# Kernel optimization log

Measured on AMD Instinct MI355X. Metric: run time of the kernel, lower is better.

The kernel has to match this reference:

```python
import jax, jax.numpy as jnp
import numpy as np

N, E = 20000, 200000
DIM, EDGE_DIM, HID = 128, 64, 256


def _linear_init(key, fan_in, fan_out):
    # torch nn.Linear default: U(-1/sqrt(fan_in), 1/sqrt(fan_in)) for W and b
    kw, kb = jax.random.split(key)
    bound = 1.0 / np.sqrt(fan_in)
    W = jax.random.uniform(kw, (fan_in, fan_out), minval=-bound, maxval=bound, dtype=jnp.float32)
    b = jax.random.uniform(kb, (fan_out,), minval=-bound, maxval=bound, dtype=jnp.float32)
    return W, b


def setup_inputs() -> dict:
    key = jax.random.key(0)
    ks = jax.random.split(key, 8)
    H = jax.random.normal(ks[0], (N, DIM), dtype=jnp.float32)
    src = jax.random.randint(ks[1], (E,), 0, N, dtype=jnp.int32)
    dst = jax.random.randint(ks[2], (E,), 0, N, dtype=jnp.int32)
    edge_index = jnp.stack([src, dst], axis=0)
    edge_attr = jax.random.normal(ks[3], (E, EDGE_DIM), dtype=jnp.float32)
    msg_W1, msg_b1 = _linear_init(ks[4], DIM + EDGE_DIM, HID)
    msg_W2, msg_b2 = _linear_init(ks[5], HID, DIM)
    self_W1, self_b1 = _linear_init(ks[6], DIM, HID)
    self_W2, self_b2 = _linear_init(ks[7], HID, DIM)
    eps = jnp.zeros((1,), dtype=jnp.float32)
    return dict(H=H, edge_index=edge_index, edge_attr=edge_attr, eps=eps,
                msg_W1=msg_W1, msg_b1=msg_b1, msg_W2=msg_W2, msg_b2=msg_b2,
                self_W1=self_W1, self_b1=self_b1, self_W2=self_W2, self_b2=self_b2)


def _mlp(x, W1, b1, W2, b2):
    h = jax.nn.relu(x @ W1 + b1)
    return h @ W2 + b2


def reference(H, edge_index, edge_attr, eps,
              msg_W1, msg_b1, msg_W2, msg_b2,
              self_W1, self_b1, self_W2, self_b2):
    src, dst = edge_index[0], edge_index[1]
    # gather source node features, concat edge features -> per-edge message MLP
    msg_in = jnp.concatenate([H[src], edge_attr], axis=-1)  # [E, dim+edge_dim]
    msg = _mlp(msg_in, msg_W1, msg_b1, msg_W2, msg_b2)       # [E, dim]
    # scatter-add messages to destination nodes
    agg = jax.ops.segment_sum(msg, dst, num_segments=H.shape[0])  # [N, dim]
    return _mlp((1.0 + eps) * H + agg, self_W1, self_b1, self_W2, self_b2)
```

## Files before the change

kernel.cpp:

```cpp
#include <hip/hip_runtime.h>

typedef float  f32x4  __attribute__((ext_vector_type(4)));
typedef short  bf16x8 __attribute__((ext_vector_type(8)));
typedef unsigned short u16;

#define NN   20000
#define NE   200000
#define DIM  128
#define EDIM 64
#define HID  256
#define KIN  192

__device__ __forceinline__ u16 f2b(float f) {
  unsigned u = __float_as_uint(f);
  u += 0x7FFFu + ((u >> 16) & 1u);
  return (u16)(u >> 16);
}

__global__ void prep_kernel(const float* __restrict__ mW1, const float* __restrict__ mW2,
                            const float* __restrict__ sW1, const float* __restrict__ sW2,
                            u16* __restrict__ W1T, u16* __restrict__ W2T,
                            u16* __restrict__ S1T, u16* __restrict__ S2T) {
  int t  = blockIdx.x * blockDim.x + threadIdx.x;
  int nt = gridDim.x * blockDim.x;
  for (int i = t; i < KIN * HID; i += nt) { int k = i / HID, n = i % HID; W1T[n * KIN + k] = f2b(mW1[i]); }
  for (int i = t; i < HID * DIM; i += nt) { int k = i / DIM, n = i % DIM; W2T[n * HID + k] = f2b(mW2[i]); }
  for (int i = t; i < DIM * HID; i += nt) { int k = i / HID, n = i % HID; S1T[n * DIM + k] = f2b(sW1[i]); }
  for (int i = t; i < HID * DIM; i += nt) { int k = i / DIM, n = i % DIM; S2T[n * HID + k] = f2b(sW2[i]); }
}

__global__ void hist_kernel(const int* __restrict__ EI, int* __restrict__ cnt) {
  int i = blockIdx.x * 256 + threadIdx.x;
  if (i < NE) atomicAdd(&cnt[EI[NE + i]], 1);
}

__global__ __launch_bounds__(1024) void scan_kernel(const int* __restrict__ cnt,
                                                    int* __restrict__ cursor) {
  __shared__ int ls[1024];
  const int t = threadIdx.x;
  const int base = t * 20;
  int v[20]; int s = 0;
  #pragma unroll
  for (int j = 0; j < 20; ++j) {
    int idx = base + j;
    int c = (idx < NN) ? cnt[idx] : 0;
    v[j] = s; s += c;
  }
  ls[t] = s;
  __syncthreads();
  for (int off = 1; off < 1024; off <<= 1) {
    int x = (t >= off) ? ls[t - off] : 0;
    __syncthreads();
    ls[t] += x;
    __syncthreads();
  }
  int boff = (t > 0) ? ls[t - 1] : 0;
  #pragma unroll
  for (int j = 0; j < 20; ++j) {
    int idx = base + j;
    if (idx < NN) cursor[idx] = boff + v[j];
  }
}

__global__ void scatter_kernel(const int* __restrict__ EI, int* __restrict__ cursor,
                               int* __restrict__ perm, int* __restrict__ srcs,
                               int* __restrict__ dsts) {
  int i = blockIdx.x * 256 + threadIdx.x;
  if (i < NE) {
    int d = EI[NE + i];
    int pos = atomicAdd(&cursor[d], 1);
    perm[pos] = i;
    srcs[pos] = EI[i];
    dsts[pos] = d;
  }
}

__global__ __launch_bounds__(256, 4) void edge_kernel(
    const float* __restrict__ H, const float* __restrict__ EA,
    const int* __restrict__ perm, const int* __restrict__ srcs,
    const int* __restrict__ dsts,
    const u16* __restrict__ W1T, const float* __restrict__ b1p,
    const u16* __restrict__ W2T, const float* __restrict__ b2p,
    float* __restrict__ agg) {
  __shared__ int src_s[64];
  __shared__ int eid_s[64];
  __shared__ int dst_s[64];
  __shared__ u16 smem[64 * HID];

  const int tid = threadIdx.x;
  const int e0  = blockIdx.x * 64;
  if (tid < 64) {
    src_s[tid] = srcs[e0 + tid];
    eid_s[tid] = perm[e0 + tid];
    dst_s[tid] = dsts[e0 + tid];
  }
  __syncthreads();

  #pragma unroll
  for (int i = 0; i < 8; ++i) {
    int idx = tid + i * 256;
    int row = idx >> 5, c4 = idx & 31;
    const float4 v = reinterpret_cast<const float4*>(H + (size_t)src_s[row] * DIM)[c4];
    int by = (c4 * 8) ^ ((row & 7) << 4);
    ushort4 o; o.x = f2b(v.x); o.y = f2b(v.y); o.z = f2b(v.z); o.w = f2b(v.w);
    *reinterpret_cast<ushort4*>(&smem[row * KIN + (by >> 1)]) = o;
  }
  #pragma unroll
  for (int i = 0; i < 4; ++i) {
    int idx = tid + i * 256;
    int row = idx >> 4, c4 = idx & 15;
    const float4 v = reinterpret_cast<const float4*>(EA + (size_t)eid_s[row] * EDIM)[c4];
    int by = (256 + c4 * 8) ^ ((row & 7) << 4);
    ushort4 o; o.x = f2b(v.x); o.y = f2b(v.y); o.z = f2b(v.z); o.w = f2b(v.w);
    *reinterpret_cast<ushort4*>(&smem[row * KIN + (by >> 1)]) = o;
  }
  __syncthreads();

  const int wv = tid >> 6, lane = tid & 63;
  const int lr = lane & 15, lg = lane >> 4;
  const f32x4 zero = {0.f, 0.f, 0.f, 0.f};

  const int n0 = wv * 64;
  f32x4 acc[4][4];
  #pragma unroll
  for (int m = 0; m < 4; ++m)
    #pragma unroll
    for (int n = 0; n < 4; ++n) acc[m][n] = zero;
  float bias1[4];
  #pragma unroll
  for (int n = 0; n < 4; ++n) bias1[n] = b1p[n0 + n * 16 + lr];

  #pragma unroll
  for (int kt = 0; kt < 6; ++kt) {
    bf16x8 af[4], bf[4];
    #pragma unroll
    for (int m = 0; m < 4; ++m) {
      int row = m * 16 + lr;
      int by  = (kt * 64 + lg * 16) ^ ((row & 7) << 4);
      af[m] = *reinterpret_cast<const bf16x8*>(&smem[row * KIN + (by >> 1)]);
    }
    #pragma unroll
    for (int n = 0; n < 4; ++n) {
      int nabs = n0 + n * 16 + lr;
      bf[n] = *reinterpret_cast<const bf16x8*>(&W1T[nabs * KIN + kt * 32 + lg * 8]);
    }
    #pragma unroll
    for (int m = 0; m < 4; ++m)
      #pragma unroll
      for (int n = 0; n < 4; ++n)
        acc[m][n] = __builtin_amdgcn_mfma_f32_16x16x32_bf16(af[m], bf[n], acc[m][n], 0, 0, 0);
  }
  __syncthreads();

  #pragma unroll
  for (int m = 0; m < 4; ++m)
    #pragma unroll
    for (int n = 0; n < 4; ++n)
      #pragma unroll
      for (int r = 0; r < 4; ++r) {
        int row = m * 16 + lg * 4 + r;
        int col = n0 + n * 16 + lr;
        float v = acc[m][n][r] + bias1[n];
        v = fmaxf(v, 0.0f);
        int by = (col * 2) ^ ((row & 7) << 4);
        smem[row * HID + (by >> 1)] = f2b(v);
      }
  __syncthreads();

  const int n0b = wv * 32;
  f32x4 acc2[4][2];
  #pragma unroll
  for (int m = 0; m < 4; ++m) { acc2[m][0] = zero; acc2[m][1] = zero; }
  float bias2[2];
  #pragma unroll
  for (int n = 0; n < 2; ++n) bias2[n] = b2p[n0b + n * 16 + lr];

  #pragma unroll
  for (int kt = 0; kt < 8; ++kt) {
    bf16x8 af[4], bf[2];
    #pragma unroll
    for (int m = 0; m < 4; ++m) {
      int row = m * 16 + lr;
      int by  = (kt * 64 + lg * 16) ^ ((row & 7) << 4);
      af[m] = *reinterpret_cast<const bf16x8*>(&smem[row * HID + (by >> 1)]);
    }
    #pragma unroll
    for (int n = 0; n < 2; ++n) {
      int nabs = n0b + n * 16 + lr;
      bf[n] = *reinterpret_cast<const bf16x8*>(&W2T[nabs * HID + kt * 32 + lg * 8]);
    }
    #pragma unroll
    for (int m = 0; m < 4; ++m)
      #pragma unroll
      for (int n = 0; n < 2; ++n)
        acc2[m][n] = __builtin_amdgcn_mfma_f32_16x16x32_bf16(af[m], bf[n], acc2[m][n], 0, 0, 0);
  }
  __syncthreads();

  float* msgf = reinterpret_cast<float*>(smem);
  #pragma unroll
  for (int m = 0; m < 4; ++m)
    #pragma unroll
    for (int n = 0; n < 2; ++n) {
      float bb = bias2[n];
      int col = n0b + n * 16 + lr;
      #pragma unroll
      for (int r = 0; r < 4; ++r) {
        int row = m * 16 + lg * 4 + r;
        msgf[row * DIM + (col ^ ((row & 7) << 2))] = acc2[m][n][r] + bb;
      }
    }
  __syncthreads();

  if (tid < DIM) {
    const int c = tid;
    float s = 0.f;
    int cur = dst_s[0];
    int seg0 = 0;
    for (int r = 0; r < 64; ++r) {
      int d = dst_s[r];
      if (d != cur) {
        if (seg0 == 0) atomicAdd(&agg[(size_t)cur * DIM + c], s);
        else           agg[(size_t)cur * DIM + c] = s;
        s = 0.f; cur = d; seg0 = r;
      }
      s += msgf[r * DIM + (c ^ ((r & 7) << 2))];
    }
    atomicAdd(&agg[(size_t)cur * DIM + c], s);
  }
}

__global__ __launch_bounds__(256, 6) void self_kernel(
    const float* __restrict__ H, const float* __restrict__ agg,
    const float* __restrict__ epsp,
    const u16* __restrict__ S1T, const float* __restrict__ b1p,
    const u16* __restrict__ S2T, const float* __restrict__ b2p,
    float* __restrict__ out) {
  __shared__ u16 smem[32 * HID];
  const int tid = threadIdx.x;
  const int r0  = blockIdx.x * 32;
  const float sc = 1.0f + epsp[0];

  #pragma unroll
  for (int i = 0; i < 4; ++i) {
    int idx = tid + i * 256;
    int row = idx >> 5, c4 = idx & 31;
    int gr = r0 + row;
    const float4 h = reinterpret_cast<const float4*>(H   + (size_t)gr * DIM)[c4];
    const float4 a = reinterpret_cast<const float4*>(agg + (size_t)gr * DIM)[c4];
    ushort4 o;
    o.x = f2b(sc * h.x + a.x); o.y = f2b(sc * h.y + a.y);
    o.z = f2b(sc * h.z + a.z); o.w = f2b(sc * h.w + a.w);
    int by = (c4 * 8) ^ ((row & 7) << 4);
    *reinterpret_cast<ushort4*>(&smem[row * DIM + (by >> 1)]) = o;
  }
  __syncthreads();

  const int wv = tid >> 6, lane = tid & 63;
  const int lr = lane & 15, lg = lane >> 4;
  const f32x4 zero = {0.f, 0.f, 0.f, 0.f};

  const int n0 = wv * 64;
  f32x4 acc[2][4];
  #pragma unroll
  for (int m = 0; m < 2; ++m)
    #pragma unroll
    for (int n = 0; n < 4; ++n) acc[m][n] = zero;
  float bias1[4];
  #pragma unroll
  for (int n = 0; n < 4; ++n) bias1[n] = b1p[n0 + n * 16 + lr];

  #pragma unroll
  for (int kt = 0; kt < 4; ++kt) {
    bf16x8 af[2], bf[4];
    #pragma unroll
    for (int m = 0; m < 2; ++m) {
      int row = m * 16 + lr;
      int by  = (kt * 64 + lg * 16) ^ ((row & 7) << 4);
      af[m] = *reinterpret_cast<const bf16x8*>(&smem[row * DIM + (by >> 1)]);
    }
    #pragma unroll
    for (int n = 0; n < 4; ++n) {
      int nabs = n0 + n * 16 + lr;
      bf[n] = *reinterpret_cast<const bf16x8*>(&S1T[nabs * DIM + kt * 32 + lg * 8]);
    }
    #pragma unroll
    for (int m = 0; m < 2; ++m)
      #pragma unroll
      for (int n = 0; n < 4; ++n)
        acc[m][n] = __builtin_amdgcn_mfma_f32_16x16x32_bf16(af[m], bf[n], acc[m][n], 0, 0, 0);
  }
  __syncthreads();

  #pragma unroll
  for (int m = 0; m < 2; ++m)
    #pragma unroll
    for (int n = 0; n < 4; ++n)
      #pragma unroll
      for (int r = 0; r < 4; ++r) {
        int row = m * 16 + lg * 4 + r;
        int col = n0 + n * 16 + lr;
        float v = acc[m][n][r] + bias1[n];
        v = fmaxf(v, 0.0f);
        int by = (col * 2) ^ ((row & 7) << 4);
        smem[row * HID + (by >> 1)] = f2b(v);
      }
  __syncthreads();

  const int n0b = wv * 32;
  f32x4 acc2[2][2];
  #pragma unroll
  for (int m = 0; m < 2; ++m) { acc2[m][0] = zero; acc2[m][1] = zero; }
  float bias2[2];
  #pragma unroll
  for (int n = 0; n < 2; ++n) bias2[n] = b2p[n0b + n * 16 + lr];

  #pragma unroll
  for (int kt = 0; kt < 8; ++kt) {
    bf16x8 af[2], bf[2];
    #pragma unroll
    for (int m = 0; m < 2; ++m) {
      int row = m * 16 + lr;
      int by  = (kt * 64 + lg * 16) ^ ((row & 7) << 4);
      af[m] = *reinterpret_cast<const bf16x8*>(&smem[row * HID + (by >> 1)]);
    }
    #pragma unroll
    for (int n = 0; n < 2; ++n) {
      int nabs = n0b + n * 16 + lr;
      bf[n] = *reinterpret_cast<const bf16x8*>(&S2T[nabs * HID + kt * 32 + lg * 8]);
    }
    #pragma unroll
    for (int m = 0; m < 2; ++m)
      #pragma unroll
      for (int n = 0; n < 2; ++n)
        acc2[m][n] = __builtin_amdgcn_mfma_f32_16x16x32_bf16(af[m], bf[n], acc2[m][n], 0, 0, 0);
  }

  #pragma unroll
  for (int m = 0; m < 2; ++m)
    #pragma unroll
    for (int n = 0; n < 2; ++n) {
      int col = n0b + n * 16 + lr;
      float bb = bias2[n];
      #pragma unroll
      for (int r = 0; r < 4; ++r) {
        int row = m * 16 + lg * 4 + r;
        int gr  = r0 + row;
        out[(size_t)gr * DIM + col] = acc2[m][n][r] + bb;
      }
    }
}

extern "C" void kernel_launch(void* const* d_in, const int* in_sizes, int n_in,
                              void* d_out, int out_size, void* d_ws, size_t ws_size,
                              hipStream_t stream) {
  const float* H   = (const float*)d_in[0];
  const int*   EI  = (const int*)  d_in[1];
  const float* EA  = (const float*)d_in[2];
  const float* EPS = (const float*)d_in[3];
  const float* mW1 = (const float*)d_in[4];
  const float* mb1 = (const float*)d_in[5];
  const float* mW2 = (const float*)d_in[6];
  const float* mb2 = (const float*)d_in[7];
  const float* sW1 = (const float*)d_in[8];
  const float* sb1 = (const float*)d_in[9];
  const float* sW2 = (const float*)d_in[10];
  const float* sb2 = (const float*)d_in[11];
  float* out = (float*)d_out;

  char* ws = (char*)d_ws;
  size_t off = 0;
  float* agg  = (float*)(ws + off); off += (size_t)NN * DIM * 4;
  int* cnt    = (int*)(ws + off); off += (size_t)NN * 4;
  int* cursor = (int*)(ws + off); off += (size_t)NN * 4;
  int* perm   = (int*)(ws + off); off += (size_t)NE * 4;
  int* srcs   = (int*)(ws + off); off += (size_t)NE * 4;
  int* dsts   = (int*)(ws + off); off += (size_t)NE * 4;
  u16* W1T = (u16*)(ws + off); off += (size_t)HID * KIN * 2;
  u16* W2T = (u16*)(ws + off); off += (size_t)DIM * HID * 2;
  u16* S1T = (u16*)(ws + off); off += (size_t)HID * DIM * 2;
  u16* S2T = (u16*)(ws + off); off += (size_t)DIM * HID * 2;

  hipMemsetAsync(agg, 0, (size_t)NN * DIM * 4, stream);
  hipMemsetAsync(cnt, 0, (size_t)NN * 4, stream);
  prep_kernel<<<96, 256, 0, stream>>>(mW1, mW2, sW1, sW2, W1T, W2T, S1T, S2T);
  hist_kernel<<<(NE + 255) / 256, 256, 0, stream>>>(EI, cnt);
  scan_kernel<<<1, 1024, 0, stream>>>(cnt, cursor);
  scatter_kernel<<<(NE + 255) / 256, 256, 0, stream>>>(EI, cursor, perm, srcs, dsts);
  edge_kernel<<<NE / 64, 256, 0, stream>>>(H, EA, perm, srcs, dsts,
                                           W1T, mb1, W2T, mb2, agg);
  self_kernel<<<NN / 32, 256, 0, stream>>>(H, agg, EPS, S1T, sb1, S2T, sb2, out);
}
```

Before: 256.9 us.

## Make edge kernel persistent with software-pipelined gather and split segment reduction

The edge kernel becomes persistent: a grid of 768 blocks loops over the 3125 64-edge tiles. While the current tile runs its MFMAs, each block prefetches the next tile's indices and its H and edge-attribute rows into registers, hiding gather latency behind compute. The segmented scatter-reduce is split across two halves of 128 threads with a boundary-merge step, so all 256 threads take part instead of 128. The two memsets are folded into the weight-prep kernel, removing separate launches; the cost is higher register pressure (launch bounds drop to 3 waves) and more complex merge logic.

```diff
diff --git a/kernel.cpp b/kernel.cpp
--- a/kernel.cpp
+++ b/kernel.cpp
@@ -10,6 +10,8 @@
 #define EDIM 64
 #define HID  256
 #define KIN  192
+#define NT   3125
+#define EGRID 768
 
 __device__ __forceinline__ u16 f2b(float f) {
   unsigned u = __float_as_uint(f);
@@ -17,12 +19,16 @@
   return (u16)(u >> 16);
 }
 
-__global__ void prep_kernel(const float* __restrict__ mW1, const float* __restrict__ mW2,
-                            const float* __restrict__ sW1, const float* __restrict__ sW2,
-                            u16* __restrict__ W1T, u16* __restrict__ W2T,
-                            u16* __restrict__ S1T, u16* __restrict__ S2T) {
+__global__ void prep_zero_kernel(const float* __restrict__ mW1, const float* __restrict__ mW2,
+                                 const float* __restrict__ sW1, const float* __restrict__ sW2,
+                                 u16* __restrict__ W1T, u16* __restrict__ W2T,
+                                 u16* __restrict__ S1T, u16* __restrict__ S2T,
+                                 float* __restrict__ agg, int* __restrict__ cnt) {
   int t  = blockIdx.x * blockDim.x + threadIdx.x;
   int nt = gridDim.x * blockDim.x;
+  float4 z = {0.f, 0.f, 0.f, 0.f};
+  for (int i = t; i < NN * DIM / 4; i += nt) reinterpret_cast<float4*>(agg)[i] = z;
+  for (int i = t; i < NN; i += nt) cnt[i] = 0;
   for (int i = t; i < KIN * HID; i += nt) { int k = i / HID, n = i % HID; W1T[n * KIN + k] = f2b(mW1[i]); }
   for (int i = t; i < HID * DIM; i += nt) { int k = i / DIM, n = i % DIM; W2T[n * HID + k] = f2b(mW2[i]); }
   for (int i = t; i < DIM * HID; i += nt) { int k = i / HID, n = i % HID; S1T[n * DIM + k] = f2b(sW1[i]); }
@@ -75,158 +81,234 @@
   }
 }
 
-__global__ __launch_bounds__(256, 4) void edge_kernel(
+__global__ __launch_bounds__(256, 3) void edge_kernel(
     const float* __restrict__ H, const float* __restrict__ EA,
     const int* __restrict__ perm, const int* __restrict__ srcs,
     const int* __restrict__ dsts,
     const u16* __restrict__ W1T, const float* __restrict__ b1p,
     const u16* __restrict__ W2T, const float* __restrict__ b2p,
     float* __restrict__ agg) {
-  __shared__ int src_s[64];
-  __shared__ int eid_s[64];
   __shared__ int dst_s[64];
+  __shared__ float lowsum[DIM];
+  __shared__ int lowstart_s;
   __shared__ u16 smem[64 * HID];
 
   const int tid = threadIdx.x;
-  const int e0  = blockIdx.x * 64;
-  if (tid < 64) {
-    src_s[tid] = srcs[e0 + tid];
-    eid_s[tid] = perm[e0 + tid];
-    dst_s[tid] = dsts[e0 + tid];
-  }
-  __syncthreads();
-
-  #pragma unroll
-  for (int i = 0; i < 8; ++i) {
-    int idx = tid + i * 256;
-    int row = idx >> 5, c4 = idx & 31;
-    const float4 v = reinterpret_cast<const float4*>(H + (size_t)src_s[row] * DIM)[c4];
-    int by = (c4 * 8) ^ ((row & 7) << 4);
-    ushort4 o; o.x = f2b(v.x); o.y = f2b(v.y); o.z = f2b(v.z); o.w = f2b(v.w);
-    *reinterpret_cast<ushort4*>(&smem[row * KIN + (by >> 1)]) = o;
-  }
-  #pragma unroll
-  for (int i = 0; i < 4; ++i) {
-    int idx = tid + i * 256;
-    int row = idx >> 4, c4 = idx & 15;
-    const float4 v = reinterpret_cast<const float4*>(EA + (size_t)eid_s[row] * EDIM)[c4];
-    int by = (256 + c4 * 8) ^ ((row & 7) << 4);
-    ushort4 o; o.x = f2b(v.x); o.y = f2b(v.y); o.z = f2b(v.z); o.w = f2b(v.w);
-    *reinterpret_cast<ushort4*>(&smem[row * KIN + (by >> 1)]) = o;
-  }
-  __syncthreads();
-
   const int wv = tid >> 6, lane = tid & 63;
   const int lr = lane & 15, lg = lane >> 4;
+  const int n0 = wv * 64, n0b = wv * 32;
   const f32x4 zero = {0.f, 0.f, 0.f, 0.f};
 
-  const int n0 = wv * 64;
-  f32x4 acc[4][4];
-  #pragma unroll
-  for (int m = 0; m < 4; ++m)
-    #pragma unroll
-    for (int n = 0; n < 4; ++n) acc[m][n] = zero;
-  float bias1[4];
+  float bias1[4], bias2[2];
   #pragma unroll
   for (int n = 0; n < 4; ++n) bias1[n] = b1p[n0 + n * 16 + lr];
-
-  #pragma unroll
-  for (int kt = 0; kt < 6; ++kt) {
-    bf16x8 af[4], bf[4];
-    #pragma unroll
-    for (int m = 0; m < 4; ++m) {
-      int row = m * 16 + lr;
-      int by  = (kt * 64 + lg * 16) ^ ((row & 7) << 4);
-      af[m] = *reinterpret_cast<const bf16x8*>(&smem[row * KIN + (by >> 1)]);
-    }
-    #pragma unroll
-    for (int n = 0; n < 4; ++n) {
-      int nabs = n0 + n * 16 + lr;
-      bf[n] = *reinterpret_cast<const bf16x8*>(&W1T[nabs * KIN + kt * 32 + lg * 8]);
-    }
+  #pragma unroll
+  for (int n = 0; n < 2; ++n) bias2[n] = b2p[n0b + n * 16 + lr];
+
+  const int hR = tid >> 5, hC = tid & 31;
+  const int eR = tid >> 4, eC = tid & 15;
+
+  {
+    const int b = blockIdx.x * 64;
+    #pragma unroll
+    for (int i = 0; i < 8; ++i) {
+      int row = hR + 8 * i;
+      int s = srcs[b + row];
+      float4 v = reinterpret_cast<const float4*>(H + (size_t)s * DIM)[hC];
+      int by = (hC * 8) ^ ((row & 7) << 4);
+      ushort4 o; o.x = f2b(v.x); o.y = f2b(v.y); o.z = f2b(v.z); o.w = f2b(v.w);
+      *reinterpret_cast<ushort4*>(&smem[row * KIN + (by >> 1)]) = o;
+    }
+    #pragma unroll
+    for (int i = 0; i < 4; ++i) {
+      int row = eR + 16 * i;
+      int e = perm[b + row];
+      float4 v = reinterpret_cast<const float4*>(EA + (size_t)e * EDIM)[eC];
+      int by = (256 + eC * 8) ^ ((row & 7) << 4);
+      ushort4 o; o.x = f2b(v.x); o.y = f2b(v.y); o.z = f2b(v.z); o.w = f2b(v.w);
+      *reinterpret_cast<ushort4*>(&smem[row * KIN + (by >> 1)]) = o;
+    }
+    if (tid < 64) dst_s[tid] = dsts[b + tid];
+  }
+  __syncthreads();
+
+  for (int t = blockIdx.x; t < NT; t += EGRID) {
+    const int tnext = t + EGRID;
+    const bool have_next = tnext < NT;
+
+    f32x4 acc[4][4];
     #pragma unroll
     for (int m = 0; m < 4; ++m)
       #pragma unroll
+      for (int n = 0; n < 4; ++n) acc[m][n] = zero;
+
+    #pragma unroll
+    for (int kt = 0; kt < 6; ++kt) {
+      bf16x8 af[4], bf[4];
+      #pragma unroll
+      for (int m = 0; m < 4; ++m) {
+        int row = m * 16 + lr;
+        int by  = (kt * 64 + lg * 16) ^ ((row & 7) << 4);
+        af[m] = *reinterpret_cast<const bf16x8*>(&smem[row * KIN + (by >> 1)]);
+      }
+      #pragma unroll
+      for (int n = 0; n < 4; ++n) {
+        int nabs = n0 + n * 16 + lr;
+        bf[n] = *reinterpret_cast<const bf16x8*>(&W1T[nabs * KIN + kt * 32 + lg * 8]);
+      }
+      #pragma unroll
+      for (int m = 0; m < 4; ++m)
+        #pragma unroll
+        for (int n = 0; n < 4; ++n)
+          acc[m][n] = __builtin_amdgcn_mfma_f32_16x16x32_bf16(af[m], bf[n], acc[m][n], 0, 0, 0);
+    }
+
+    int hsrcn[8], heidn[4], dnext = 0;
+    if (have_next) {
+      const int nb = tnext * 64;
+      #pragma unroll
+      for (int i = 0; i < 8; ++i) hsrcn[i] = srcs[nb + hR + 8 * i];
+      #pragma unroll
+      for (int i = 0; i < 4; ++i) heidn[i] = perm[nb + eR + 16 * i];
+      if (tid < 64) dnext = dsts[nb + tid];
+    }
+    __syncthreads();
+
+    #pragma unroll
+    for (int m = 0; m < 4; ++m)
+      #pragma unroll
       for (int n = 0; n < 4; ++n)
-        acc[m][n] = __builtin_amdgcn_mfma_f32_16x16x32_bf16(af[m], bf[n], acc[m][n], 0, 0, 0);
-  }
-  __syncthreads();
-
-  #pragma unroll
-  for (int m = 0; m < 4; ++m)
-    #pragma unroll
-    for (int n = 0; n < 4; ++n)
-      #pragma unroll
-      for (int r = 0; r < 4; ++r) {
-        int row = m * 16 + lg * 4 + r;
-        int col = n0 + n * 16 + lr;
-        float v = acc[m][n][r] + bias1[n];
-        v = fmaxf(v, 0.0f);
-        int by = (col * 2) ^ ((row & 7) << 4);
-        smem[row * HID + (by >> 1)] = f2b(v);
-      }
-  __syncthreads();
-
-  const int n0b = wv * 32;
-  f32x4 acc2[4][2];
-  #pragma unroll
-  for (int m = 0; m < 4; ++m) { acc2[m][0] = zero; acc2[m][1] = zero; }
-  float bias2[2];
-  #pragma unroll
-  for (int n = 0; n < 2; ++n) bias2[n] = b2p[n0b + n * 16 + lr];
-
-  #pragma unroll
-  for (int kt = 0; kt < 8; ++kt) {
-    bf16x8 af[4], bf[2];
-    #pragma unroll
-    for (int m = 0; m < 4; ++m) {
-      int row = m * 16 + lr;
-      int by  = (kt * 64 + lg * 16) ^ ((row & 7) << 4);
-      af[m] = *reinterpret_cast<const bf16x8*>(&smem[row * HID + (by >> 1)]);
-    }
-    #pragma unroll
-    for (int n = 0; n < 2; ++n) {
-      int nabs = n0b + n * 16 + lr;
-      bf[n] = *reinterpret_cast<const bf16x8*>(&W2T[nabs * HID + kt * 32 + lg * 8]);
-    }
+        #pragma unroll
+        for (int r = 0; r < 4; ++r) {
+          int row = m * 16 + lg * 4 + r;
+          int col = n0 + n * 16 + lr;
+          float v = acc[m][n][r] + bias1[n];
+          v = fmaxf(v, 0.0f);
+          int by = (col * 2) ^ ((row & 7) << 4);
+          smem[row * HID + (by >> 1)] = f2b(v);
+        }
+    __syncthreads();
+
+    f32x4 acc2[4][2];
+    #pragma unroll
+    for (int m = 0; m < 4; ++m) { acc2[m][0] = zero; acc2[m][1] = zero; }
+
+    #pragma unroll
+    for (int kt = 0; kt < 8; ++kt) {
+      bf16x8 af[4], bf[2];
+      #pragma unroll
+      for (int m = 0; m < 4; ++m) {
+        int row = m * 16 + lr;
+        int by  = (kt * 64 + lg * 16) ^ ((row & 7) << 4);
+        af[m] = *reinterpret_cast<const bf16x8*>(&smem[row * HID + (by >> 1)]);
+      }
+      #pragma unroll
+      for (int n = 0; n < 2; ++n) {
+        int nabs = n0b + n * 16 + lr;
+        bf[n] = *reinterpret_cast<const bf16x8*>(&W2T[nabs * HID + kt * 32 + lg * 8]);
+      }
+      #pragma unroll
+      for (int m = 0; m < 4; ++m)
+        #pragma unroll
+        for (int n = 0; n < 2; ++n)
+          acc2[m][n] = __builtin_amdgcn_mfma_f32_16x16x32_bf16(af[m], bf[n], acc2[m][n], 0, 0, 0);
+    }
+    __syncthreads();
+
+    float4 hvn[8], evn[4];
+    if (have_next) {
+      #pragma unroll
+      for (int i = 0; i < 8; ++i)
+        hvn[i] = reinterpret_cast<const float4*>(H + (size_t)hsrcn[i] * DIM)[hC];
+      #pragma unroll
+      for (int i = 0; i < 4; ++i)
+        evn[i] = reinterpret_cast<const float4*>(EA + (size_t)heidn[i] * EDIM)[eC];
+    }
+
+    float* msgf = reinterpret_cast<float*>(smem);
     #pragma unroll
     for (int m = 0; m < 4; ++m)
       #pragma unroll
-      for (int n = 0; n < 2; ++n)
-        acc2[m][n] = __builtin_amdgcn_mfma_f32_16x16x32_bf16(af[m], bf[n], acc2[m][n], 0, 0, 0);
-  }
-  __syncthreads();
-
-  float* msgf = reinterpret_cast<float*>(smem);
-  #pragma unroll
-  for (int m = 0; m < 4; ++m)
-    #pragma unroll
-    for (int n = 0; n < 2; ++n) {
-      float bb = bias2[n];
-      int col = n0b + n * 16 + lr;
-      #pragma unroll
-      for (int r = 0; r < 4; ++r) {
-        int row = m * 16 + lg * 4 + r;
-        msgf[row * DIM + (col ^ ((row & 7) << 2))] = acc2[m][n][r] + bb;
-      }
-    }
-  __syncthreads();
-
-  if (tid < DIM) {
-    const int c = tid;
-    float s = 0.f;
-    int cur = dst_s[0];
-    int seg0 = 0;
-    for (int r = 0; r < 64; ++r) {
-      int d = dst_s[r];
-      if (d != cur) {
-        if (seg0 == 0) atomicAdd(&agg[(size_t)cur * DIM + c], s);
-        else           agg[(size_t)cur * DIM + c] = s;
-        s = 0.f; cur = d; seg0 = r;
-      }
-      s += msgf[r * DIM + (c ^ ((r & 7) << 2))];
-    }
-    atomicAdd(&agg[(size_t)cur * DIM + c], s);
+      for (int n = 0; n < 2; ++n) {
+        float bb = bias2[n];
+        int col = n0b + n * 16 + lr;
+        #pragma unroll
+        for (int r = 0; r < 4; ++r) {
+          int row = m * 16 + lg * 4 + r;
+          msgf[row * DIM + (col ^ ((row & 7) << 2))] = acc2[m][n][r] + bb;
+        }
+      }
+    __syncthreads();
+
+    const int c = tid & 127;
+    int cur, segstart; float s;
+    bool first = true; float fsum = 0.f; int fdst = 0;
+    int d31 = 0; bool cont = false;
+    if (tid < 128) {
+      cur = dst_s[0]; segstart = 0;
+      s = msgf[0 * DIM + c];
+      for (int r = 1; r < 32; ++r) {
+        int d = dst_s[r];
+        if (d != cur) {
+          if (segstart == 0) atomicAdd(&agg[(size_t)cur * DIM + c], s);
+          else               agg[(size_t)cur * DIM + c] = s;
+          s = 0.f; cur = d; segstart = r;
+        }
+        s += msgf[r * DIM + (c ^ ((r & 7) << 2))];
+      }
+      lowsum[c] = s;
+      if (tid == 0) lowstart_s = segstart;
+    } else {
+      d31 = dst_s[31];
+      cur = dst_s[32]; cont = (cur == d31); segstart = 32;
+      s = msgf[32 * DIM + c];
+      for (int r = 33; r < 64; ++r) {
+        int d = dst_s[r];
+        if (d != cur) {
+          if (first) { fsum = s; fdst = cur; first = false; }
+          else       agg[(size_t)cur * DIM + c] = s;
+          s = 0.f; cur = d; segstart = r;
+        }
+        s += msgf[r * DIM + (c ^ ((r & 7) << 2))];
+      }
+    }
+    __syncthreads();
+
+    if (tid >= 128) {
+      if (!cont) {
+        float ls = lowsum[c];
+        if (lowstart_s == 0) atomicAdd(&agg[(size_t)d31 * DIM + c], ls);
+        else                 agg[(size_t)d31 * DIM + c] = ls;
+      }
+      if (first) {
+        atomicAdd(&agg[(size_t)cur * DIM + c], s + (cont ? lowsum[c] : 0.f));
+      } else {
+        float v = fsum + (cont ? lowsum[c] : 0.f);
+        int fstart = cont ? lowstart_s : 32;
+        if (fstart == 0) atomicAdd(&agg[(size_t)fdst * DIM + c], v);
+        else             agg[(size_t)fdst * DIM + c] = v;
+        atomicAdd(&agg[(size_t)cur * DIM + c], s);
+      }
+    }
+
+    if (have_next) {
+      #pragma unroll
+      for (int i = 0; i < 8; ++i) {
+        int row = hR + 8 * i;
+        int by = (hC * 8) ^ ((row & 7) << 4);
+        ushort4 o; o.x = f2b(hvn[i].x); o.y = f2b(hvn[i].y); o.z = f2b(hvn[i].z); o.w = f2b(hvn[i].w);
+        *reinterpret_cast<ushort4*>(&smem[row * KIN + (by >> 1)]) = o;
+      }
+      #pragma unroll
+      for (int i = 0; i < 4; ++i) {
+        int row = eR + 16 * i;
+        int by = (256 + eC * 8) ^ ((row & 7) << 4);
+        ushort4 o; o.x = f2b(evn[i].x); o.y = f2b(evn[i].y); o.z = f2b(evn[i].z); o.w = f2b(evn[i].w);
+        *reinterpret_cast<ushort4*>(&smem[row * KIN + (by >> 1)]) = o;
+      }
+      if (tid < 64) dst_s[tid] = dnext;
+    }
+    __syncthreads();
   }
 }
 
@@ -381,13 +463,11 @@
   u16* S1T = (u16*)(ws + off); off += (size_t)HID * DIM * 2;
   u16* S2T = (u16*)(ws + off); off += (size_t)DIM * HID * 2;
 
-  hipMemsetAsync(agg, 0, (size_t)NN * DIM * 4, stream);
-  hipMemsetAsync(cnt, 0, (size_t)NN * 4, stream);
-  prep_kernel<<<96, 256, 0, stream>>>(mW1, mW2, sW1, sW2, W1T, W2T, S1T, S2T);
+  prep_zero_kernel<<<640, 256, 0, stream>>>(mW1, mW2, sW1, sW2, W1T, W2T, S1T, S2T, agg, cnt);
   hist_kernel<<<(NE + 255) / 256, 256, 0, stream>>>(EI, cnt);
   scan_kernel<<<1, 1024, 0, stream>>>(cnt, cursor);
   scatter_kernel<<<(NE + 255) / 256, 256, 0, stream>>>(EI, cursor, perm, srcs, dsts);
-  edge_kernel<<<NE / 64, 256, 0, stream>>>(H, EA, perm, srcs, dsts,
-                                           W1T, mb1, W2T, mb2, agg);
+  edge_kernel<<<EGRID, 256, 0, stream>>>(H, EA, perm, srcs, dsts,
+                                         W1T, mb1, W2T, mb2, agg);
   self_kernel<<<NN / 32, 256, 0, stream>>>(H, agg, EPS, S1T, sb1, S2T, sb2, out);
 }
```

New measurement: 541.9 us. 111% more time.
